# Kernel tuning notes

Measured on AMD Instinct MI355X. Metric: run time of the kernel, lower is better.

The kernel has to match this reference:

```python
import jax, jax.numpy as jnp
import numpy as np

B, D, N = 1024, 2048, 30000
IOU_CLIP_LO, IOU_CLIP_HI = 0.2, 0.9


def _l2norm(x, axis=-1, eps=1e-12):
    return x / jnp.maximum(jnp.linalg.norm(x, axis=axis, keepdims=True), eps)


def setup_inputs() -> dict:
    key = jax.random.key(0)
    k1, k2, k3, k4, k5 = jax.random.split(key, 5)
    inputs = _l2norm(jax.random.normal(k1, (B, D), jnp.float32))
    features = _l2norm(jax.random.normal(k2, (N, D), jnp.float32))
    IoU = jax.random.uniform(k3, (B,), jnp.float32)
    indexes = jax.random.randint(k4, (B,), 0, N, dtype=jnp.int64)
    update_flag = jax.random.randint(k5, (B,), 0, 2, dtype=jnp.int32)
    return {"inputs": inputs, "features": features, "IoU": IoU,
            "indexes": indexes, "update_flag": update_flag}


def reference(inputs, features, IoU, indexes, update_flag):
    # Forward of HM.apply: similarity logits vs memory bank.
    outputs = inputs @ features.T  # [B, N]

    # Memory-bank update (side effect performed in HM.backward), update_method='max_iou':
    # sequential per-row conditional overwrite + L2 renorm; duplicates in `indexes`
    # must be processed in order, hence lax.scan.
    iou_c = jnp.clip(IoU, IOU_CLIP_LO, IOU_CLIP_HI)  # clamped as in backward (unused by max_iou)

    def step(feats, xs):
        x, y, iou, uf = xs
        row = feats[y]
        row = jnp.where(uf > 0, x, row)          # max_iou: overwrite if update_flag
        row = row / jnp.maximum(jnp.linalg.norm(row), 1e-12)  # row renorm (always)
        return feats.at[y].set(row), None

    new_features, _ = jax.lax.scan(step, features, (inputs, indexes, iou_c, update_flag))
    return outputs, new_features
```

## Files before the change

kernel.cpp:

```cpp
#include <hip/hip_runtime.h>
#include <stdint.h>

#define B_ROWS 1024
#define DDIM   2048
#define NFEAT  30000

#define BM 256
#define BN 256
#define BK 64
#define GRID_M 4
#define GRID_N 118
#define NBLOCKS (GRID_M * GRID_N)
#define NKT (DDIM / BK)

typedef __attribute__((ext_vector_type(8))) short short8;
typedef __attribute__((ext_vector_type(4))) float v4f;

typedef const __attribute__((address_space(1))) unsigned int* gptr_t;
typedef __attribute__((address_space(3))) unsigned int* lptr_t;

__device__ __forceinline__ unsigned short f32_to_bf16(float f) {
    unsigned int u = __float_as_uint(f);
    unsigned int r = u + 0x7FFFu + ((u >> 16) & 1u);
    return (unsigned short)(r >> 16);
}

__device__ __forceinline__ void async_copy16(const void* g, void* l) {
    __builtin_amdgcn_global_load_lds((gptr_t)g, (lptr_t)l, 16, 0, 0);
}

__global__ void f32_to_bf16_kernel(const float4* __restrict__ src,
                                   ushort4* __restrict__ dst, int n4) {
    int stride = gridDim.x * blockDim.x;
    for (int i = blockIdx.x * blockDim.x + threadIdx.x; i < n4; i += stride) {
        float4 v = src[i];
        ushort4 o;
        o.x = f32_to_bf16(v.x);
        o.y = f32_to_bf16(v.y);
        o.z = f32_to_bf16(v.z);
        o.w = f32_to_bf16(v.w);
        dst[i] = o;
    }
}

__global__ void fused_feat_kernel(const float4* __restrict__ src,
                                  ushort4* __restrict__ dstB,
                                  float4* __restrict__ dstF, int n4) {
    int stride = gridDim.x * blockDim.x;
    for (int i = blockIdx.x * blockDim.x + threadIdx.x; i < n4; i += stride) {
        float4 v = src[i];
        dstF[i] = v;
        ushort4 o;
        o.x = f32_to_bf16(v.x);
        o.y = f32_to_bf16(v.y);
        o.z = f32_to_bf16(v.z);
        o.w = f32_to_bf16(v.w);
        dstB[i] = o;
    }
}

__global__ void copy_f32_kernel(const float4* __restrict__ src,
                                float4* __restrict__ dst, int n4) {
    int stride = gridDim.x * blockDim.x;
    for (int i = blockIdx.x * blockDim.x + threadIdx.x; i < n4; i += stride) {
        dst[i] = src[i];
    }
}

__global__ __launch_bounds__(512, 2) void gemm_bf16_8ph(
    const unsigned short* __restrict__ A,
    const unsigned short* __restrict__ Bf,
    float* __restrict__ C)
{
    __shared__ alignas(16) unsigned char lds[131072];

    const int tid  = threadIdx.x;
    const int wave = tid >> 6;
    const int lane = tid & 63;
    const int wm   = wave >> 2;
    const int wn   = wave & 3;
    const int bh   = wn >> 1;

    const int bid  = blockIdx.x;
    const int wgid = (bid & 7) * (NBLOCKS / 8) + (bid >> 3);
    const int mblk = wgid & (GRID_M - 1);
    const int nblk = wgid >> 2;

    const unsigned char* Ab = (const unsigned char*)A;
    const unsigned char* Bb = (const unsigned char*)Bf;

    size_t a_src[2][2], b_src[2][2];
    int ld_off[2];
#pragma unroll
    for (int j = 0; j < 2; ++j) {
        const int P = (wave + j * 8) * 1024 + lane * 16;
        const int Q = P ^ (((P >> 9) & 1) << 5);
        const int kh  = Q >> 13;
        const int row = (Q >> 6) & 127;
        const int cb  = Q & 63;
        ld_off[j] = (wave + j * 8) * 1024;
#pragma unroll
        for (int h = 0; h < 2; ++h) {
            const int ga = mblk * BM + h * 128 + row;
            int gb = nblk * BN + h * 128 + row;
            if (gb >= NFEAT) gb = NFEAT - 1;
            a_src[h][j] = (size_t)ga * (DDIM * 2) + kh * 64 + cb;
            b_src[h][j] = (size_t)gb * (DDIM * 2) + kh * 64 + cb;
        }
    }

#define STAGE_A(kt, h) do {                                                         \
    unsigned char* _d = &lds[((((kt) & 1) * 2 + (h)) << 14)];                       \
    async_copy16(Ab + a_src[h][0] + (size_t)(kt) * 128, _d + ld_off[0]);            \
    async_copy16(Ab + a_src[h][1] + (size_t)(kt) * 128, _d + ld_off[1]);            \
} while (0)

#define STAGE_B(kt, h) do {                                                         \
    unsigned char* _d = &lds[65536 + ((((kt) & 1) * 2 + (h)) << 14)];               \
    async_copy16(Bb + b_src[h][0] + (size_t)(kt) * 128, _d + ld_off[0]);            \
    async_copy16(Bb + b_src[h][1] + (size_t)(kt) * 128, _d + ld_off[1]);            \
} while (0)

    int aoff[4], boff[4];
#pragma unroll
    for (int j = 0; j < 4; ++j) {
        const int ar = j * 32 + wm * 16 + (lane & 15);
        const int aq = ar * 64 + (lane >> 4) * 16;
        aoff[j] = aq ^ (((ar >> 3) & 1) << 5);
        const int br = (wn & 1) * 64 + j * 16 + (lane & 15);
        const int bq = br * 64 + (lane >> 4) * 16;
        boff[j] = bq ^ (((br >> 3) & 1) << 5);
    }

#define READ_A(slot, f, ks) \
    (*(const short8*)&lds[((((slot) * 2) + ((f) >> 2)) << 14) + (ks) * 8192 + aoff[(f) & 3]])
#define READ_B(slot, n, ks) \
    (*(const short8*)&lds[65536 + ((((slot) * 2) + bh) << 14) + (ks) * 8192 + boff[n]])

    v4f acc[8][4];
#pragma unroll
    for (int f = 0; f < 8; ++f)
#pragma unroll
        for (int n = 0; n < 4; ++n)
            acc[f][n] = (v4f){0.f, 0.f, 0.f, 0.f};

    short8 af[2][2];
    short8 bfr[4][2];

#define MFMA_QUAD(f0) do {                                                                             \
    _Pragma("unroll")                                                                                  \
    for (int n = 0; n < 4; ++n) {                                                                      \
        acc[(f0)][n]     = __builtin_amdgcn_mfma_f32_16x16x32_bf16(af[0][0], bfr[n][0], acc[(f0)][n],     0, 0, 0); \
        acc[(f0)][n]     = __builtin_amdgcn_mfma_f32_16x16x32_bf16(af[0][1], bfr[n][1], acc[(f0)][n],     0, 0, 0); \
        acc[(f0) + 1][n] = __builtin_amdgcn_mfma_f32_16x16x32_bf16(af[1][0], bfr[n][0], acc[(f0) + 1][n], 0, 0, 0); \
        acc[(f0) + 1][n] = __builtin_amdgcn_mfma_f32_16x16x32_bf16(af[1][1], bfr[n][1], acc[(f0) + 1][n], 0, 0, 0); \
    }                                                                                                  \
} while (0)

    STAGE_B(0, 0); STAGE_B(0, 1); STAGE_A(0, 0); STAGE_A(0, 1);
    STAGE_B(1, 0); STAGE_B(1, 1); STAGE_A(1, 0);
    asm volatile("s_waitcnt vmcnt(6)" ::: "memory");
    __builtin_amdgcn_s_barrier();

    for (int t = 0; t < NKT; ++t) {
        const int slot = t & 1;

        af[0][0] = READ_A(slot, 0, 0); af[0][1] = READ_A(slot, 0, 1);
        af[1][0] = READ_A(slot, 1, 0); af[1][1] = READ_A(slot, 1, 1);
#pragma unroll
        for (int n = 0; n < 4; ++n) {
            bfr[n][0] = READ_B(slot, n, 0);
            bfr[n][1] = READ_B(slot, n, 1);
        }
        if (t + 1 < NKT) STAGE_A(t + 1, 1);
        asm volatile("s_waitcnt lgkmcnt(8)" ::: "memory");
        __builtin_amdgcn_s_barrier();
        asm volatile("s_waitcnt lgkmcnt(0)" ::: "memory");
        __builtin_amdgcn_s_setprio(1);
        MFMA_QUAD(0);
        __builtin_amdgcn_s_setprio(0);
        __builtin_amdgcn_s_barrier();

        af[0][0] = READ_A(slot, 2, 0); af[0][1] = READ_A(slot, 2, 1);
        af[1][0] = READ_A(slot, 3, 0); af[1][1] = READ_A(slot, 3, 1);
        if (t + 2 < NKT) STAGE_B(t + 2, 0);
        __builtin_amdgcn_s_barrier();
        asm volatile("s_waitcnt lgkmcnt(0)" ::: "memory");
        __builtin_amdgcn_s_setprio(1);
        MFMA_QUAD(2);
        __builtin_amdgcn_s_setprio(0);
        __builtin_amdgcn_s_barrier();

        af[0][0] = READ_A(slot, 4, 0); af[0][1] = READ_A(slot, 4, 1);
        af[1][0] = READ_A(slot, 5, 0); af[1][1] = READ_A(slot, 5, 1);
        if (t + 2 < NKT) STAGE_B(t + 2, 1);
        __builtin_amdgcn_s_barrier();
        asm volatile("s_waitcnt lgkmcnt(0)" ::: "memory");
        __builtin_amdgcn_s_setprio(1);
        MFMA_QUAD(4);
        __builtin_amdgcn_s_setprio(0);
        __builtin_amdgcn_s_barrier();

        af[0][0] = READ_A(slot, 6, 0); af[0][1] = READ_A(slot, 6, 1);
        af[1][0] = READ_A(slot, 7, 0); af[1][1] = READ_A(slot, 7, 1);
        if (t + 2 < NKT) STAGE_A(t + 2, 0);
        __builtin_amdgcn_s_barrier();
        asm volatile("s_waitcnt lgkmcnt(0)" ::: "memory");
        __builtin_amdgcn_s_setprio(1);
        MFMA_QUAD(6);
        __builtin_amdgcn_s_setprio(0);
        if (t < NKT - 2) {
            asm volatile("s_waitcnt vmcnt(6)" ::: "memory");
        } else if (t == NKT - 2) {
            asm volatile("s_waitcnt vmcnt(0)" ::: "memory");
        }
        __builtin_amdgcn_s_barrier();
    }

#pragma unroll
    for (int f = 0; f < 8; ++f) {
        const int gr = mblk * BM + f * 32 + wm * 16 + (lane >> 4) * 4;
#pragma unroll
        for (int n = 0; n < 4; ++n) {
            const int gc = nblk * BN + wn * 64 + n * 16 + (lane & 15);
            if (gc < NFEAT) {
#pragma unroll
                for (int r = 0; r < 4; ++r)
                    C[(size_t)(gr + r) * NFEAT + gc] = acc[f][n][r];
            }
        }
    }
#undef STAGE_A
#undef STAGE_B
#undef READ_A
#undef READ_B
#undef MFMA_QUAD
}

__global__ void scatter_rows_kernel(const float* __restrict__ inputs,
                                    const int* __restrict__ idx,
                                    const int* __restrict__ uf,
                                    float* __restrict__ out_feats) {
    int b = blockIdx.x;
    if (uf[b] <= 0) return;
    int y = idx[b];
    __shared__ int dead;
    if (threadIdx.x == 0) dead = 0;
    __syncthreads();
    for (int b2 = b + 1 + threadIdx.x; b2 < B_ROWS; b2 += blockDim.x) {
        if (uf[b2] > 0 && idx[b2] == y) { dead = 1; break; }
    }
    __syncthreads();
    if (dead) return;
    const float4* s = (const float4*)(inputs + (size_t)b * DDIM);
    float4* d = (float4*)(out_feats + (size_t)y * DDIM);
    for (int i = threadIdx.x; i < DDIM / 4; i += blockDim.x) d[i] = s[i];
}

extern "C" void kernel_launch(void* const* d_in, const int* in_sizes, int n_in,
                              void* d_out, int out_size, void* d_ws, size_t ws_size,
                              hipStream_t stream) {
    const float* inputs   = (const float*)d_in[0];
    const float* features = (const float*)d_in[1];
    const int* indexes    = (const int*)d_in[3];
    const int* uf         = (const int*)d_in[4];

    float* out0 = (float*)d_out;
    float* out1 = out0 + (size_t)B_ROWS * NFEAT;

    const int nf4 = NFEAT * DDIM / 4;
    const int na4 = B_ROWS * DDIM / 4;

    const size_t featB_bytes = (size_t)NFEAT * DDIM * 2;
    const size_t inpB_bytes  = (size_t)B_ROWS * DDIM * 2;

    if (d_ws && ws_size >= featB_bytes + inpB_bytes) {
        unsigned short* featB = (unsigned short*)d_ws;
        unsigned short* inpB  = (unsigned short*)((char*)d_ws + featB_bytes);

        fused_feat_kernel<<<4096, 256, 0, stream>>>((const float4*)features,
                                                    (ushort4*)featB, (float4*)out1, nf4);
        f32_to_bf16_kernel<<<2048, 256, 0, stream>>>((const float4*)inputs, (ushort4*)inpB, na4);
        gemm_bf16_8ph<<<NBLOCKS, 512, 0, stream>>>(inpB, featB, out0);
        scatter_rows_kernel<<<B_ROWS, 256, 0, stream>>>(inputs, indexes, uf, out1);
    } else {
        unsigned short* featB = (unsigned short*)out1;
        unsigned short* inpB  = featB + (size_t)NFEAT * DDIM;

        f32_to_bf16_kernel<<<8192, 256, 0, stream>>>((const float4*)features, (ushort4*)featB, nf4);
        f32_to_bf16_kernel<<<2048, 256, 0, stream>>>((const float4*)inputs, (ushort4*)inpB, na4);
        gemm_bf16_8ph<<<NBLOCKS, 512, 0, stream>>>(inpB, featB, out0);
        copy_f32_kernel<<<8192, 256, 0, stream>>>((const float4*)features, (float4*)out1, nf4);
        scatter_rows_kernel<<<B_ROWS, 256, 0, stream>>>(inputs, indexes, uf, out1);
    }
}
```

Baseline: 670.9 us.

## Use row-contiguous LDS layout with XOR swizzle and nontemporal feature copy

Reorganizes the GEMM's LDS tile layout so that each row holds a full 128-byte K-slice with an XOR swizzle on 16-byte chunks, in place of the earlier split into two 64-byte K halves. The global loads now read whole contiguous 128-byte row segments, and the fragment reads are remapped to match. Both changes are meant to reduce LDS bank conflicts and improve global coalescing. Separately, the fused feature conversion kernel uses nontemporal loads and stores to avoid polluting caches with the streamed fp32 copy. The risk is that a mismatch between the swizzle and the reads would give wrong results, and that nontemporal hints may change how L2 handles the bf16 data later reused by the GEMM.

```diff
diff --git a/kernel.cpp b/kernel.cpp
--- a/kernel.cpp
+++ b/kernel.cpp
@@ -15,6 +15,7 @@
 
 typedef __attribute__((ext_vector_type(8))) short short8;
 typedef __attribute__((ext_vector_type(4))) float v4f;
+typedef __attribute__((ext_vector_type(4))) unsigned short u16x4;
 
 typedef const __attribute__((address_space(1))) unsigned int* gptr_t;
 typedef __attribute__((address_space(3))) unsigned int* lptr_t;
@@ -43,14 +44,14 @@
     }
 }
 
-__global__ void fused_feat_kernel(const float4* __restrict__ src,
-                                  ushort4* __restrict__ dstB,
-                                  float4* __restrict__ dstF, int n4) {
+__global__ void fused_feat_kernel(const v4f* __restrict__ src,
+                                  u16x4* __restrict__ dstB,
+                                  v4f* __restrict__ dstF, int n4) {
     int stride = gridDim.x * blockDim.x;
     for (int i = blockIdx.x * blockDim.x + threadIdx.x; i < n4; i += stride) {
-        float4 v = src[i];
-        dstF[i] = v;
-        ushort4 o;
+        v4f v = __builtin_nontemporal_load(&src[i]);
+        __builtin_nontemporal_store(v, &dstF[i]);
+        u16x4 o;
         o.x = f32_to_bf16(v.x);
         o.y = f32_to_bf16(v.y);
         o.z = f32_to_bf16(v.z);
@@ -93,19 +94,17 @@
     int ld_off[2];
 #pragma unroll
     for (int j = 0; j < 2; ++j) {
-        const int P = (wave + j * 8) * 1024 + lane * 16;
-        const int Q = P ^ (((P >> 9) & 1) << 5);
-        const int kh  = Q >> 13;
-        const int row = (Q >> 6) & 127;
-        const int cb  = Q & 63;
-        ld_off[j] = (wave + j * 8) * 1024;
+        const int chunk = wave + j * 8;
+        ld_off[j] = chunk * 1024;
+        const int rrow = chunk * 8 + (lane >> 3);
+        const int cb   = (((lane & 7) ^ (lane >> 3)) * 16);
 #pragma unroll
         for (int h = 0; h < 2; ++h) {
-            const int ga = mblk * BM + h * 128 + row;
-            int gb = nblk * BN + h * 128 + row;
+            const int ga = mblk * BM + h * 128 + rrow;
+            int gb = nblk * BN + h * 128 + rrow;
             if (gb >= NFEAT) gb = NFEAT - 1;
-            a_src[h][j] = (size_t)ga * (DDIM * 2) + kh * 64 + cb;
-            b_src[h][j] = (size_t)gb * (DDIM * 2) + kh * 64 + cb;
+            a_src[h][j] = (size_t)ga * (DDIM * 2) + cb;
+            b_src[h][j] = (size_t)gb * (DDIM * 2) + cb;
         }
     }
 
@@ -121,21 +120,24 @@
     async_copy16(Bb + b_src[h][1] + (size_t)(kt) * 128, _d + ld_off[1]);            \
 } while (0)
 
-    int aoff[4], boff[4];
+    int aoff[4][2], boff[4][2];
 #pragma unroll
     for (int j = 0; j < 4; ++j) {
-        const int ar = j * 32 + wm * 16 + (lane & 15);
-        const int aq = ar * 64 + (lane >> 4) * 16;
-        aoff[j] = aq ^ (((ar >> 3) & 1) << 5);
-        const int br = (wn & 1) * 64 + j * 16 + (lane & 15);
-        const int bq = br * 64 + (lane >> 4) * 16;
-        boff[j] = bq ^ (((br >> 3) & 1) << 5);
+#pragma unroll
+        for (int ks = 0; ks < 2; ++ks) {
+            const int ar = j * 32 + wm * 16 + (lane & 15);
+            const int as = ((lane >> 4) + 4 * ks) ^ (ar & 7);
+            aoff[j][ks] = ar * 128 + as * 16;
+            const int br = (wn & 1) * 64 + j * 16 + (lane & 15);
+            const int bs = ((lane >> 4) + 4 * ks) ^ (br & 7);
+            boff[j][ks] = br * 128 + bs * 16;
+        }
     }
 
 #define READ_A(slot, f, ks) \
-    (*(const short8*)&lds[((((slot) * 2) + ((f) >> 2)) << 14) + (ks) * 8192 + aoff[(f) & 3]])
+    (*(const short8*)&lds[((((slot) * 2) + ((f) >> 2)) << 14) + aoff[(f) & 3][ks]])
 #define READ_B(slot, n, ks) \
-    (*(const short8*)&lds[65536 + ((((slot) * 2) + bh) << 14) + (ks) * 8192 + boff[n]])
+    (*(const short8*)&lds[65536 + ((((slot) * 2) + bh) << 14) + boff[n][ks]])
 
     v4f acc[8][4];
 #pragma unroll
@@ -278,8 +280,8 @@
         unsigned short* featB = (unsigned short*)d_ws;
         unsigned short* inpB  = (unsigned short*)((char*)d_ws + featB_bytes);
 
-        fused_feat_kernel<<<4096, 256, 0, stream>>>((const float4*)features,
-                                                    (ushort4*)featB, (float4*)out1, nf4);
+        fused_feat_kernel<<<4096, 256, 0, stream>>>((const v4f*)features,
+                                                    (u16x4*)featB, (v4f*)out1, nf4);
         f32_to_bf16_kernel<<<2048, 256, 0, stream>>>((const float4*)inputs, (ushort4*)inpB, na4);
         gemm_bf16_8ph<<<NBLOCKS, 512, 0, stream>>>(inpB, featB, out0);
         scatter_rows_kernel<<<B_ROWS, 256, 0, stream>>>(inputs, indexes, uf, out1);
```

Measured after the change: 648.4 us. 1.03x faster.
